# Kernel optimization log

Hardware: AMD Instinct MI355X
Metric: run time of the kernel (lower is better)

## Reference

```python
import jax, jax.numpy as jnp
import numpy as np

D_MODEL = 1024
N_HEADS = 16
D_HEAD = D_MODEL // N_HEADS
D_FF = 4096
EPS = 1e-5
NEG = -1e10


def setup_inputs() -> dict:
    key = jax.random.key(0)
    ks = jax.random.split(key, 16)
    s = 0.02
    x = jax.random.normal(ks[0], (4, 1024, D_MODEL), dtype=jnp.float32)
    mask = jnp.ones((4, 1, 1, 1024), dtype=jnp.int32)
    return {
        "x": x,
        "mask": mask,
        "Wq": jax.random.normal(ks[1], (D_MODEL, D_MODEL), jnp.float32) * s,
        "Wk": jax.random.normal(ks[2], (D_MODEL, D_MODEL), jnp.float32) * s,
        "Wv": jax.random.normal(ks[3], (D_MODEL, D_MODEL), jnp.float32) * s,
        "Wp": jax.random.normal(ks[4], (D_MODEL, D_MODEL), jnp.float32) * s,
        "bp": jnp.zeros((D_MODEL,), jnp.float32),
        "W1": jax.random.normal(ks[5], (D_MODEL, D_FF), jnp.float32) * s,
        "b1": jnp.zeros((D_FF,), jnp.float32),
        "W2": jax.random.normal(ks[6], (D_FF, D_MODEL), jnp.float32) * s,
        "b2": jnp.zeros((D_MODEL,), jnp.float32),
        "g1": jnp.ones((D_MODEL,), jnp.float32),
        "be1": jnp.zeros((D_MODEL,), jnp.float32),
        "g2": jnp.ones((D_MODEL,), jnp.float32),
        "be2": jnp.zeros((D_MODEL,), jnp.float32),
    }


def _layer_norm(x, g, b):
    mu = jnp.mean(x, axis=-1, keepdims=True)
    var = jnp.mean(jnp.square(x - mu), axis=-1, keepdims=True)
    return (x - mu) * jax.lax.rsqrt(var + EPS) * g + b


def _mha(x, mask, Wq, Wk, Wv, Wp, bp):
    B, L, _ = x.shape
    q = (x @ Wq).reshape(B, L, N_HEADS, D_HEAD).transpose(0, 2, 1, 3)  # (B,H,L,dh)
    k = (x @ Wk).reshape(B, L, N_HEADS, D_HEAD).transpose(0, 2, 1, 3)
    v = (x @ Wv).reshape(B, L, N_HEADS, D_HEAD).transpose(0, 2, 1, 3)
    scores = jnp.einsum('bhqd,bhkd->bhqk', q, k) / jnp.sqrt(jnp.float32(D_HEAD))
    scores = jnp.where(mask == 0, NEG, scores)
    attn = jax.nn.softmax(scores, axis=-1)
    heads = jnp.einsum('bhqk,bhkd->bhqd', attn, v)  # (B,H,L,dh)
    heads = heads.transpose(0, 2, 1, 3).reshape(B, L, D_MODEL)
    return heads @ Wp + bp


def reference(x, mask, Wq, Wk, Wv, Wp, bp, W1, b1, W2, b2, g1, be1, g2, be2):
    # Post-norm residual sublayers (dropout inactive at inference)
    attn_out = _mha(x, mask, Wq, Wk, Wv, Wp, bp)
    h = _layer_norm(x + attn_out, g1, be1)
    ff = jax.nn.relu(h @ W1 + b1) @ W2 + b2
    out = _layer_norm(h + ff, g2, be2)
    return out
```

## Files before the change

### kernel.cpp

```cpp
#include <hip/hip_runtime.h>
#include <hip/hip_bf16.h>

typedef __attribute__((ext_vector_type(8))) short short8;
typedef __attribute__((ext_vector_type(4))) short short4v;
typedef __attribute__((ext_vector_type(4))) float float4v;

static __device__ __forceinline__ float b2f(short s) {
    return __builtin_bit_cast(float, ((unsigned)(unsigned short)s) << 16);
}
static __device__ __forceinline__ short f2b(float f) {
    unsigned x = __builtin_bit_cast(unsigned, f);
    unsigned r = (x + 0x7fffu + ((x >> 16) & 1u)) >> 16;
    return (short)r;
}
static __device__ __forceinline__ void gload_lds16(const short* g, short* l) {
    __builtin_amdgcn_global_load_lds(
        (const __attribute__((address_space(1))) void*)g,
        (__attribute__((address_space(3))) void*)l, 16, 0, 0);
}

static __device__ __forceinline__ void tile_transpose(const float* __restrict__ in,
                                                      short* __restrict__ out,
                                                      int R, int C, int bx, int by,
                                                      float tile[64][65])
{
    const int tx = threadIdx.x;
    const int r0 = by * 64, c0 = bx * 64;
    const int lr = tx >> 4, lc = (tx & 15) * 4;
#pragma unroll
    for (int p = 0; p < 4; p++) {
        const float4v v = *(const float4v*)&in[(size_t)(r0 + lr + p * 16) * C + c0 + lc];
#pragma unroll
        for (int j = 0; j < 4; j++) tile[lr + p * 16][lc + j] = v[j];
    }
    __syncthreads();
    const int oc = tx >> 3, orr = (tx & 7) * 8;
#pragma unroll
    for (int p = 0; p < 2; p++) {
        const int c = oc + p * 32;
        short8 pk;
#pragma unroll
        for (int j = 0; j < 8; j++) pk[j] = f2b(tile[orr + j][c]);
        *(short8*)&out[(size_t)(c0 + c) * R + r0 + orr] = pk;
    }
}

__global__ __launch_bounds__(256) void prep_k(const float* __restrict__ x,
                                              const float* __restrict__ Wq,
                                              const float* __restrict__ Wk,
                                              const float* __restrict__ Wv,
                                              const float* __restrict__ Wp,
                                              const float* __restrict__ W1,
                                              const float* __restrict__ W2,
                                              short* __restrict__ xb,
                                              short* __restrict__ WqkvT,
                                              short* __restrict__ WpT,
                                              short* __restrict__ W1T,
                                              short* __restrict__ W2T)
{
    __shared__ float tile[64][65];
    const int b = blockIdx.x;
    if (b < 4096) {
        const size_t i = ((size_t)b * 256 + threadIdx.x) * 4;
        const float4v v = *(const float4v*)&x[i];
        short4v s;
#pragma unroll
        for (int j = 0; j < 4; j++) s[j] = f2b(v[j]);
        *(short4v*)&xb[i] = s;
    } else if (b < 5120) {
        const int lb = b - 4096;
        const int wsel = lb >> 8, t = lb & 255;
        const float* in = (wsel == 0) ? Wq : (wsel == 1) ? Wk : (wsel == 2) ? Wv : Wp;
        short* out = (wsel < 3) ? (WqkvT + ((size_t)wsel << 20)) : WpT;
        tile_transpose(in, out, 1024, 1024, t & 15, t >> 4, tile);
    } else if (b < 6144) {
        const int lb = b - 5120;
        tile_transpose(W1, W1T, 1024, 4096, lb & 63, lb >> 6, tile);
    } else {
        const int lb = b - 6144;
        tile_transpose(W2, W2T, 4096, 1024, lb & 15, lb >> 4, tile);
    }
}

template<int MODE, int BM, int BN, int KH, int MM, int NN, int KK, int SPLIT>
__global__ __launch_bounds__(256) void gemm_bt(const short* __restrict__ X,
                                               const short* __restrict__ Wt,
                                               short* __restrict__ out,
                                               const float* __restrict__ bias,
                                               const short* __restrict__ alt)
{
    constexpr int MI = BM / 32, NI = BN / 32;
    constexpr int BK = KH * 32;
    constexpr int NT = (KK / SPLIT) / BK;
    __shared__ short As[KH][BM * 32];
    __shared__ short Bs[KH][BN * 32];
    const int tid = threadIdx.x;
    const int wave = tid >> 6, lane = tid & 63;
    const int quad = lane >> 4, l16 = lane & 15;

    int bx = blockIdx.x, by = blockIdx.y;
    {
        constexpr int nbx = NN / BN, nby = MM / BM;
        if ((nby & 7) == 0) {
            const int g = by * nbx + bx;
            const int xcd = g & 7, local = g >> 3, Y = nby >> 3;
            by = xcd * Y + (local % Y);
            bx = local / Y;
        }
    }
    const int m0 = by * BM, n0 = bx * BN;
    const int wm = (wave >> 1) * (BM / 2), wn = (wave & 1) * (BN / 2);

    int kb = 0;
    short* op = out;
    if (MODE == 5) {
        kb = blockIdx.z * (KK / SPLIT);
        op = (blockIdx.z == SPLIT - 1 && alt) ? const_cast<short*>(alt)
                                              : out + (size_t)blockIdx.z * MM * NN;
    }

    const int srow = tid >> 2;
    const int scs = (((tid & 3) ^ (srow & 3)) * 8);
    const int rg = ((l16 & 3)) * 8;

    const short* ap = X + (size_t)(m0 + srow) * KK + kb + scs;
    const short* bp = Wt + (size_t)(n0 + srow) * KK + kb + scs;

    float4v acc[MI][NI] = {};

    for (int it = 0; it < NT; ++it) {
#pragma unroll
        for (int c = 0; c < BM / 64; c++)
#pragma unroll
            for (int h = 0; h < KH; h++)
                gload_lds16(ap + (size_t)c * 64 * KK + h * 32, &As[h][(c * 256 + tid) * 8]);
#pragma unroll
        for (int c = 0; c < BN / 64; c++)
#pragma unroll
            for (int h = 0; h < KH; h++)
                gload_lds16(bp + (size_t)c * 64 * KK + h * 32, &Bs[h][(c * 256 + tid) * 8]);
        ap += BK; bp += BK;
        __syncthreads();
#pragma unroll
        for (int h = 0; h < KH; h++) {
            short8 af[MI], bf[NI];
#pragma unroll
            for (int i = 0; i < MI; i++)
                af[i] = *(const short8*)&As[h][(wm + i * 16 + l16) * 32 + ((quad * 8) ^ rg)];
#pragma unroll
            for (int i = 0; i < NI; i++)
                bf[i] = *(const short8*)&Bs[h][(wn + i * 16 + l16) * 32 + ((quad * 8) ^ rg)];
#pragma unroll
            for (int mi = 0; mi < MI; mi++)
#pragma unroll
                for (int ni = 0; ni < NI; ni++)
                    acc[mi][ni] = __builtin_amdgcn_mfma_f32_16x16x32_bf16(af[mi], bf[ni], acc[mi][ni], 0, 0, 0);
        }
        __syncthreads();
    }

#pragma unroll
    for (int mi = 0; mi < MI; mi++) {
#pragma unroll
        for (int ni = 0; ni < NI; ni++) {
            const int gn = n0 + wn + ni * 16 + l16;
            const float bv = (MODE == 2) ? bias[gn] : 0.0f;
#pragma unroll
            for (int r = 0; r < 4; r++) {
                const int gm = m0 + wm + mi * 16 + quad * 4 + r;
                float v = acc[mi][ni][r];
                if (MODE == 4) {
                    const int s = gn >> 10;
                    const int n = gn & 1023;
                    const int hh = n >> 6, d = n & 63;
                    const size_t bh16 = (size_t)((gm >> 10) * 16 + hh) << 16;
                    const size_t base = (size_t)s << 22;
                    if (s == 0)      out[base + bh16 + ((size_t)(gm & 1023) << 6) + d] = f2b(v * 0.125f);
                    else if (s == 1) out[base + bh16 + ((size_t)(gm & 1023) << 6) + d] = f2b(v);
                    else             out[base + bh16 + ((size_t)d << 10) + (gm & 1023)] = f2b(v);
                } else if (MODE == 2) {
                    v += bv;
                    v = fmaxf(v, 0.0f);
                    out[(size_t)gm * NN + gn] = f2b(v);
                } else {
                    op[(size_t)gm * NN + gn] = f2b(v);
                }
            }
        }
    }
}

__global__ __launch_bounds__(256) void attn_k(const short* __restrict__ Qb,
                                              const short* __restrict__ Kb,
                                              const short* __restrict__ Vt,
                                              const int* __restrict__ mask,
                                              short* __restrict__ heads)
{
    __shared__ short Kl[2][64 * 32];
    __shared__ short Vl[2][64 * 32];
    __shared__ short P[4][16 * 72];
    const int bh = blockIdx.x, qb = blockIdx.y;
    const int b = bh >> 4, h = bh & 15;
    const int tid = threadIdx.x, wave = tid >> 6, lane = tid & 63;
    const int quad = lane >> 4, l16 = lane & 15;
    const int qbase = qb * 64 + wave * 16;
    const short* Qp = Qb + ((size_t)bh << 16) + (size_t)qbase * 64;
    const short* Kp = Kb + ((size_t)bh << 16);
    const short* Vp = Vt + ((size_t)bh << 16);
    const int* mp = mask + (b << 10);

    const short8 bq0 = *(const short8*)&Qp[l16 * 64 + quad * 8];
    const short8 bq1 = *(const short8*)&Qp[l16 * 64 + 32 + quad * 8];

    float rs = 0.0f;
    float4v o[4] = {};
    short* myP = &P[wave][0];

    const int srow = tid >> 2, sc8 = (tid & 3) * 8;

    gload_lds16(Kp + (size_t)srow * 64 + sc8,        &Kl[0][tid * 8]);
    gload_lds16(Kp + (size_t)srow * 64 + 32 + sc8,   &Kl[1][tid * 8]);
    gload_lds16(Vp + (size_t)srow * 1024 + sc8,      &Vl[0][tid * 8]);
    gload_lds16(Vp + (size_t)srow * 1024 + 32 + sc8, &Vl[1][tid * 8]);

    for (int kc = 0; kc < 1024; kc += 64) {
        __syncthreads();

        short8 nk0, nk1, nv0, nv1;
        const bool pf = (kc + 64) < 1024;
        if (pf) {
            const int kn = kc + 64;
            nk0 = *(const short8*)&Kp[(size_t)(kn + srow) * 64 + sc8];
            nk1 = *(const short8*)&Kp[(size_t)(kn + srow) * 64 + 32 + sc8];
            nv0 = *(const short8*)&Vp[(size_t)srow * 1024 + kn + sc8];
            nv1 = *(const short8*)&Vp[(size_t)srow * 1024 + kn + 32 + sc8];
        }

        float4v s[4];
#pragma unroll
        for (int kt = 0; kt < 4; kt++) {
            s[kt] = (float4v){};
            const short8 ka = *(const short8*)&Kl[0][(kt * 16 + l16) * 32 + quad * 8];
            s[kt] = __builtin_amdgcn_mfma_f32_16x16x32_bf16(ka, bq0, s[kt], 0, 0, 0);
            const short8 kb = *(const short8*)&Kl[1][(kt * 16 + l16) * 32 + quad * 8];
            s[kt] = __builtin_amdgcn_mfma_f32_16x16x32_bf16(kb, bq1, s[kt], 0, 0, 0);
        }
#pragma unroll
        for (int kt = 0; kt < 4; kt++) {
            const int4 mv = *(const int4*)&mp[kc + kt * 16 + quad * 4];
            float p0 = mv.x ? __expf(fminf(s[kt][0], 30.f)) : 0.f;
            float p1 = mv.y ? __expf(fminf(s[kt][1], 30.f)) : 0.f;
            float p2 = mv.z ? __expf(fminf(s[kt][2], 30.f)) : 0.f;
            float p3 = mv.w ? __expf(fminf(s[kt][3], 30.f)) : 0.f;
            rs += (p0 + p1) + (p2 + p3);
            short4v w;
            w[0] = f2b(p0); w[1] = f2b(p1); w[2] = f2b(p2); w[3] = f2b(p3);
            *(short4v*)&myP[l16 * 72 + kt * 16 + quad * 4] = w;
        }
        const short8 bp0 = *(const short8*)&myP[l16 * 72 + quad * 8];
        const short8 bp1 = *(const short8*)&myP[l16 * 72 + 32 + quad * 8];
#pragma unroll
        for (int dt = 0; dt < 4; dt++) {
            const short8 va = *(const short8*)&Vl[0][(dt * 16 + l16) * 32 + quad * 8];
            o[dt] = __builtin_amdgcn_mfma_f32_16x16x32_bf16(va, bp0, o[dt], 0, 0, 0);
            const short8 vb = *(const short8*)&Vl[1][(dt * 16 + l16) * 32 + quad * 8];
            o[dt] = __builtin_amdgcn_mfma_f32_16x16x32_bf16(vb, bp1, o[dt], 0, 0, 0);
        }

        __syncthreads();
        if (pf) {
            *(short8*)&Kl[0][tid * 8] = nk0;
            *(short8*)&Kl[1][tid * 8] = nk1;
            *(short8*)&Vl[0][tid * 8] = nv0;
            *(short8*)&Vl[1][tid * 8] = nv1;
        }
    }

    rs += __shfl_xor(rs, 16);
    rs += __shfl_xor(rs, 32);
    const float inv = 1.0f / fmaxf(rs, 1e-20f);
    const int gq = qbase + l16;
#pragma unroll
    for (int dt = 0; dt < 4; dt++) {
        short4v w;
#pragma unroll
        for (int r = 0; r < 4; r++) w[r] = f2b(o[dt][r] * inv);
        *(short4v*)&heads[((size_t)(b * 1024 + gq) << 10) + h * 64 + dt * 16 + quad * 4] = w;
    }
}

template<int NP, bool F32OUT>
__global__ __launch_bounds__(256) void red_ln_k(const short* __restrict__ p0,
                                                const short* __restrict__ p1,
                                                const short* __restrict__ p2,
                                                const short* __restrict__ p3,
                                                const float* __restrict__ bias,
                                                const short* __restrict__ res,
                                                const float* __restrict__ g,
                                                const float* __restrict__ be,
                                                short* __restrict__ outb,
                                                float* __restrict__ outf)
{
    __shared__ float red[8];
    const int row = blockIdx.x, tid = threadIdx.x;
    const size_t base = ((size_t)row << 10) + tid * 4;
    const short4v a = *(const short4v*)&p0[base];
    const short4v b = *(const short4v*)&p1[base];
    const short4v e = *(const short4v*)&res[base];
    const float4v bv = *(const float4v*)&bias[tid * 4];
    float v[4];
#pragma unroll
    for (int i = 0; i < 4; i++) v[i] = b2f(a[i]) + b2f(b[i]) + bv[i] + b2f(e[i]);
    if constexpr (NP == 4) {
        const short4v c = *(const short4v*)&p2[base];
        const short4v d = *(const short4v*)&p3[base];
#pragma unroll
        for (int i = 0; i < 4; i++) v[i] += b2f(c[i]) + b2f(d[i]);
    }
    float s = v[0] + v[1] + v[2] + v[3];
#pragma unroll
    for (int off = 32; off; off >>= 1) s += __shfl_xor(s, off);
    if ((tid & 63) == 0) red[tid >> 6] = s;
    __syncthreads();
    const float mu = (red[0] + red[1] + red[2] + red[3]) * (1.0f / 1024.0f);
    float vs = 0.f;
#pragma unroll
    for (int i = 0; i < 4; i++) { const float dd = v[i] - mu; vs += dd * dd; }
#pragma unroll
    for (int off = 32; off; off >>= 1) vs += __shfl_xor(vs, off);
    if ((tid & 63) == 0) red[4 + (tid >> 6)] = vs;
    __syncthreads();
    const float rstd = rsqrtf((red[4] + red[5] + red[6] + red[7]) * (1.0f / 1024.0f) + 1e-5f);
    const float4v gv = *(const float4v*)&g[tid * 4];
    const float4v bev = *(const float4v*)&be[tid * 4];
    if (F32OUT) {
        float4v w;
#pragma unroll
        for (int i = 0; i < 4; i++) w[i] = (v[i] - mu) * rstd * gv[i] + bev[i];
        *(float4v*)&outf[base] = w;
    } else {
        short4v w;
#pragma unroll
        for (int i = 0; i < 4; i++) w[i] = f2b((v[i] - mu) * rstd * gv[i] + bev[i]);
        *(short4v*)&outb[base] = w;
    }
}

extern "C" void kernel_launch(void* const* d_in, const int* in_sizes, int n_in,
                              void* d_out, int out_size, void* d_ws, size_t ws_size,
                              hipStream_t stream)
{
    const float* x   = (const float*)d_in[0];
    const int*   mk  = (const int*)d_in[1];
    const float* Wq  = (const float*)d_in[2];
    const float* Wk  = (const float*)d_in[3];
    const float* Wv  = (const float*)d_in[4];
    const float* Wp  = (const float*)d_in[5];
    const float* bp  = (const float*)d_in[6];
    const float* W1  = (const float*)d_in[7];
    const float* b1  = (const float*)d_in[8];
    const float* W2  = (const float*)d_in[9];
    const float* b2  = (const float*)d_in[10];
    const float* g1  = (const float*)d_in[11];
    const float* be1 = (const float*)d_in[12];
    const float* g2  = (const float*)d_in[13];
    const float* be2 = (const float*)d_in[14];
    float* out = (float*)d_out;

    char* ws = (char*)d_ws;
    const size_t MB = (size_t)1 << 20;
    short* xb     = (short*)(ws + 0 * MB);
    short* WqkvT  = (short*)(ws + 8 * MB);
    short* WpT    = (short*)(ws + 14 * MB);
    short* W1T    = (short*)(ws + 16 * MB);
    short* W2T    = (short*)(ws + 24 * MB);
    short* Qb     = (short*)(ws + 32 * MB);
    short* Kb     = (short*)(ws + 40 * MB);
    short* Vt     = (short*)(ws + 48 * MB);
    short* hd     = (short*)(ws + 56 * MB);
    short* partP  = (short*)(ws + 32 * MB);
    short* u      = (short*)(ws + 32 * MB);
    short* partF  = (short*)(ws + 0 * MB);
    short* partF3 = (short*)(ws + 64 * MB);
    short* hbuf   = (short*)(ws + 72 * MB);

    const dim3 blk(256);

    prep_k<<<dim3(7168), blk, 0, stream>>>(x, Wq, Wk, Wv, Wp, W1, W2,
                                           xb, WqkvT, WpT, W1T, W2T);

    gemm_bt<4, 128, 64, 2, 4096, 3072, 1024, 1>
        <<<dim3(48, 32), blk, 0, stream>>>(xb, WqkvT, Qb, nullptr, nullptr);

    attn_k<<<dim3(64, 16), blk, 0, stream>>>(Qb, Kb, Vt, mk, hd);

    gemm_bt<5, 128, 64, 2, 4096, 1024, 1024, 2>
        <<<dim3(16, 32, 2), blk, 0, stream>>>(hd, WpT, partP, nullptr, nullptr);

    red_ln_k<2, false><<<dim3(4096), blk, 0, stream>>>(partP, partP + (4u << 20), nullptr, nullptr,
                                                       bp, xb, g1, be1, hbuf, nullptr);

    gemm_bt<2, 128, 128, 2, 4096, 4096, 1024, 1>
        <<<dim3(32, 32), blk, 0, stream>>>(hbuf, W1T, u, b1, nullptr);

    gemm_bt<5, 128, 128, 2, 4096, 1024, 4096, 4>
        <<<dim3(8, 32, 4), blk, 0, stream>>>(u, W2T, partF, nullptr, partF3);

    red_ln_k<4, true><<<dim3(4096), blk, 0, stream>>>(partF, partF + (4u << 20), partF + (8u << 20), partF3,
                                                      b2, hbuf, g2, be2, nullptr, out);
}
```

Measured before the change: 329.9 us.

## Read K/V directly from global memory in attention and reorder grid

The attention kernel drops its LDS staging of K and V tiles, along with the two block barriers per iteration, and has each wave load its MFMA operands straight from global memory. The grid is also transposed so that consecutive blocks share the same batch-head and can reuse K/V through L2. This removes the synchronisation and LDS traffic, but every one of the four waves now fetches the same K/V data from global/L2 with no software prefetch. Load latency is therefore exposed, and performance depends on cache hits.

```diff
diff --git a/kernel.cpp b/kernel.cpp
--- a/kernel.cpp
+++ b/kernel.cpp
@@ -196,10 +196,8 @@
                                               const int* __restrict__ mask,
                                               short* __restrict__ heads)
 {
-    __shared__ short Kl[2][64 * 32];
-    __shared__ short Vl[2][64 * 32];
     __shared__ short P[4][16 * 72];
-    const int bh = blockIdx.x, qb = blockIdx.y;
+    const int qb = blockIdx.x, bh = blockIdx.y;
     const int b = bh >> 4, h = bh & 15;
     const int tid = threadIdx.x, wave = tid >> 6, lane = tid & 63;
     const int quad = lane >> 4, l16 = lane & 15;
@@ -216,33 +214,14 @@
     float4v o[4] = {};
     short* myP = &P[wave][0];
 
-    const int srow = tid >> 2, sc8 = (tid & 3) * 8;
-
-    gload_lds16(Kp + (size_t)srow * 64 + sc8,        &Kl[0][tid * 8]);
-    gload_lds16(Kp + (size_t)srow * 64 + 32 + sc8,   &Kl[1][tid * 8]);
-    gload_lds16(Vp + (size_t)srow * 1024 + sc8,      &Vl[0][tid * 8]);
-    gload_lds16(Vp + (size_t)srow * 1024 + 32 + sc8, &Vl[1][tid * 8]);
-
     for (int kc = 0; kc < 1024; kc += 64) {
-        __syncthreads();
-
-        short8 nk0, nk1, nv0, nv1;
-        const bool pf = (kc + 64) < 1024;
-        if (pf) {
-            const int kn = kc + 64;
-            nk0 = *(const short8*)&Kp[(size_t)(kn + srow) * 64 + sc8];
-            nk1 = *(const short8*)&Kp[(size_t)(kn + srow) * 64 + 32 + sc8];
-            nv0 = *(const short8*)&Vp[(size_t)srow * 1024 + kn + sc8];
-            nv1 = *(const short8*)&Vp[(size_t)srow * 1024 + kn + 32 + sc8];
-        }
-
         float4v s[4];
 #pragma unroll
         for (int kt = 0; kt < 4; kt++) {
             s[kt] = (float4v){};
-            const short8 ka = *(const short8*)&Kl[0][(kt * 16 + l16) * 32 + quad * 8];
+            const short8 ka = *(const short8*)&Kp[(size_t)(kc + kt * 16 + l16) * 64 + quad * 8];
             s[kt] = __builtin_amdgcn_mfma_f32_16x16x32_bf16(ka, bq0, s[kt], 0, 0, 0);
-            const short8 kb = *(const short8*)&Kl[1][(kt * 16 + l16) * 32 + quad * 8];
+            const short8 kb = *(const short8*)&Kp[(size_t)(kc + kt * 16 + l16) * 64 + 32 + quad * 8];
             s[kt] = __builtin_amdgcn_mfma_f32_16x16x32_bf16(kb, bq1, s[kt], 0, 0, 0);
         }
 #pragma unroll
@@ -261,18 +240,10 @@
         const short8 bp1 = *(const short8*)&myP[l16 * 72 + 32 + quad * 8];
 #pragma unroll
         for (int dt = 0; dt < 4; dt++) {
-            const short8 va = *(const short8*)&Vl[0][(dt * 16 + l16) * 32 + quad * 8];
+            const short8 va = *(const short8*)&Vp[(size_t)(dt * 16 + l16) * 1024 + kc + quad * 8];
             o[dt] = __builtin_amdgcn_mfma_f32_16x16x32_bf16(va, bp0, o[dt], 0, 0, 0);
-            const short8 vb = *(const short8*)&Vl[1][(dt * 16 + l16) * 32 + quad * 8];
+            const short8 vb = *(const short8*)&Vp[(size_t)(dt * 16 + l16) * 1024 + kc + 32 + quad * 8];
             o[dt] = __builtin_amdgcn_mfma_f32_16x16x32_bf16(vb, bp1, o[dt], 0, 0, 0);
-        }
-
-        __syncthreads();
-        if (pf) {
-            *(short8*)&Kl[0][tid * 8] = nk0;
-            *(short8*)&Kl[1][tid * 8] = nk1;
-            *(short8*)&Vl[0][tid * 8] = nv0;
-            *(short8*)&Vl[1][tid * 8] = nv1;
         }
     }
 
@@ -392,7 +363,7 @@
     gemm_bt<4, 128, 64, 2, 4096, 3072, 1024, 1>
         <<<dim3(48, 32), blk, 0, stream>>>(xb, WqkvT, Qb, nullptr, nullptr);
 
-    attn_k<<<dim3(64, 16), blk, 0, stream>>>(Qb, Kb, Vt, mk, hd);
+    attn_k<<<dim3(16, 64), blk, 0, stream>>>(Qb, Kb, Vt, mk, hd);
 
     gemm_bt<5, 128, 64, 2, 4096, 1024, 1024, 2>
         <<<dim3(16, 32, 2), blk, 0, stream>>>(hd, WpT, partP, nullptr, nullptr);
```

Result: slower. 417.0 us (+26.4%).
